# Kernel optimization log

Measured on AMD Instinct MI355X. Metric: run time of the kernel, lower is better.

The kernel has to match this reference:

```python
import jax, jax.numpy as jnp
import numpy as np

WIN = 11      # window_size in pytorch_msssim
SIGMA = 1.5   # gaussian sigma in create_window
LEVELS = 5


def _gauss_window(channels, dtype):
    # 1D gaussian -> normalized 2D window, replicated per channel for depthwise conv
    x = jnp.arange(WIN, dtype=dtype) - WIN // 2
    g = jnp.exp(-(x * x) / (2.0 * SIGMA * SIGMA))
    g = g / jnp.sum(g)
    w2 = jnp.outer(g, g)  # [11,11]
    return jnp.broadcast_to(w2[None, None], (channels, 1, WIN, WIN))


def _dwconv(x, w):
    # depthwise valid conv, NCHW (matches F.conv2d(..., padding=0, groups=channel))
    return jax.lax.conv_general_dilated(
        x, w, window_strides=(1, 1), padding='VALID',
        dimension_numbers=('NCHW', 'OIHW', 'NCHW'),
        feature_group_count=x.shape[1])


def _ssim_cs(p, t, w):
    # pytorch_msssim.ssim with full=True, val_range L=1 (inputs in [0,1])
    C1 = 0.01 ** 2
    C2 = 0.03 ** 2
    mu1 = _dwconv(p, w)
    mu2 = _dwconv(t, w)
    mu1_sq = mu1 * mu1
    mu2_sq = mu2 * mu2
    mu1_mu2 = mu1 * mu2
    sigma1_sq = _dwconv(p * p, w) - mu1_sq
    sigma2_sq = _dwconv(t * t, w) - mu2_sq
    sigma12 = _dwconv(p * t, w) - mu1_mu2
    v1 = 2.0 * sigma12 + C2
    v2 = sigma1_sq + sigma2_sq + C2
    # per-category means (axis 1 = the 10 categories, batched as channels)
    cs = jnp.mean(v1 / v2, axis=(0, 2, 3))                                   # [C]
    sim = jnp.mean(((2.0 * mu1_mu2 + C1) * v1) / ((mu1_sq + mu2_sq + C1) * v2),
                   axis=(0, 2, 3))                                           # [C]
    return sim, cs


def _avg_pool2(x):
    n, c, h, w = x.shape
    return x.reshape(n, c, h // 2, 2, w // 2, 2).mean(axis=(3, 5))


def setup_inputs() -> dict:
    key = jax.random.key(0)
    k1, k2 = jax.random.split(key)
    y_pred = jax.random.uniform(k1, (10, 1024, 1024), dtype=jnp.float32)
    y_true = jax.random.uniform(k2, (10, 1024, 1024), dtype=jnp.float32)
    return {"y_pred": y_pred, "y_true": y_true}


def reference(y_pred, y_true):
    # MSSLoss.forward: loss = sum over 10 categories of msssim(pred[c], true[c]);
    # return 1 - mean(loss)  (loss is a scalar, so mean is identity).
    # All 10 per-category msssim calls are batched as channels of one depthwise conv.
    dtype = y_pred.dtype
    weights = jnp.array([0.0448, 0.2856, 0.3001, 0.2363, 0.1333], dtype=dtype)
    p = y_pred[None]  # [1,10,H,W]
    t = y_true[None]
    w = _gauss_window(p.shape[1], dtype)
    sims, css = [], []
    for _ in range(LEVELS):
        s, c = _ssim_cs(p, t, w)
        sims.append(s)
        css.append(c)
        p = _avg_pool2(p)
        t = _avg_pool2(t)
    mssim = jnp.stack(sims)  # [5, 10]
    mcs = jnp.stack(css)     # [5, 10]
    pow1 = mcs ** weights[:, None]
    pow2 = mssim ** weights[:, None]
    # Po-Hsun-Su pytorch_msssim: output = torch.prod(pow1[:-1] * pow2[-1])
    per_cat = jnp.prod(pow1[:-1] * pow2[-1][None, :], axis=0)  # [10]
    return 1.0 - jnp.sum(per_cat)
```

## Files before the change

### kernel.cpp

```cpp
#include <hip/hip_runtime.h>
#include <cstddef>

#define WIN 11
#define HALO 10
#define NCH 10

typedef float v4f __attribute__((ext_vector_type(4)));

constexpr float Gc[WIN] = {
    0.00102838f, 0.00759876f, 0.03600077f, 0.10936069f, 0.21300554f,
    0.26601173f, 0.21300554f, 0.10936069f, 0.03600077f, 0.00759876f,
    0.00102838f};

constexpr int HPITCH = 33;
constexpr int RS = 76;
constexpr int RSZ = RS * HPITCH;

struct Ptrs {
    const float* p[5];
    const float* t[5];
};

__global__ __launch_bounds__(256) void pool_all(
    const float* __restrict__ P0, const float* __restrict__ T0,
    float* __restrict__ p1, float* __restrict__ t1,
    float* __restrict__ p2, float* __restrict__ t2,
    float* __restrict__ p3, float* __restrict__ t3,
    float* __restrict__ p4, float* __restrict__ t4,
    float* __restrict__ acc) {
    __shared__ float sp2[256], st2[256], sp3[64], st3[64];
    const int tid = threadIdx.x;
    if (blockIdx.x == 0 && tid < 128) acc[tid] = 0.f;

    const int b = blockIdx.x;
    const int bx = b & 15, by = (b >> 4) & 15, ch = b >> 8;
    const int tx = tid & 15, ty = tid >> 4;

    const size_t rbase =
        ((size_t)ch * 1024 + by * 64 + ty * 4) * 1024 + bx * 64 + tx * 4;
    float4 pr[4], tr[4];
#pragma unroll
    for (int r2 = 0; r2 < 4; ++r2) {
        pr[r2] = *(const float4*)(P0 + rbase + (size_t)r2 * 1024);
        tr[r2] = *(const float4*)(T0 + rbase + (size_t)r2 * 1024);
    }
    float p1a = 0.25f * ((pr[0].x + pr[0].y) + (pr[1].x + pr[1].y));
    float p1b = 0.25f * ((pr[0].z + pr[0].w) + (pr[1].z + pr[1].w));
    float p1c = 0.25f * ((pr[2].x + pr[2].y) + (pr[3].x + pr[3].y));
    float p1d = 0.25f * ((pr[2].z + pr[2].w) + (pr[3].z + pr[3].w));
    float t1a = 0.25f * ((tr[0].x + tr[0].y) + (tr[1].x + tr[1].y));
    float t1b = 0.25f * ((tr[0].z + tr[0].w) + (tr[1].z + tr[1].w));
    float t1c = 0.25f * ((tr[2].x + tr[2].y) + (tr[3].x + tr[3].y));
    float t1d = 0.25f * ((tr[2].z + tr[2].w) + (tr[3].z + tr[3].w));
    size_t o1 = ((size_t)ch * 512 + by * 32 + ty * 2) * 512 + bx * 32 + tx * 2;
    *(float2*)(p1 + o1) = make_float2(p1a, p1b);
    *(float2*)(p1 + o1 + 512) = make_float2(p1c, p1d);
    *(float2*)(t1 + o1) = make_float2(t1a, t1b);
    *(float2*)(t1 + o1 + 512) = make_float2(t1c, t1d);
    float p2v = 0.25f * ((p1a + p1b) + (p1c + p1d));
    float t2v = 0.25f * ((t1a + t1b) + (t1c + t1d));
    size_t o2 = ((size_t)ch * 256 + by * 16 + ty) * 256 + bx * 16 + tx;
    p2[o2] = p2v;
    t2[o2] = t2v;
    sp2[tid] = p2v;
    st2[tid] = t2v;
    __syncthreads();
    if (tid < 64) {
        int x3 = tid & 7, y3 = tid >> 3;
        int i0 = (2 * y3) * 16 + 2 * x3;
        float p3v = 0.25f * ((sp2[i0] + sp2[i0 + 1]) + (sp2[i0 + 16] + sp2[i0 + 17]));
        float t3v = 0.25f * ((st2[i0] + st2[i0 + 1]) + (st2[i0 + 16] + st2[i0 + 17]));
        size_t o3 = ((size_t)ch * 128 + by * 8 + y3) * 128 + bx * 8 + x3;
        p3[o3] = p3v;
        t3[o3] = t3v;
        sp3[tid] = p3v;
        st3[tid] = t3v;
    }
    __syncthreads();
    if (tid < 16) {
        int x4 = tid & 3, y4 = tid >> 2;
        int i0 = (2 * y4) * 8 + 2 * x4;
        float p4v = 0.25f * ((sp3[i0] + sp3[i0 + 1]) + (sp3[i0 + 8] + sp3[i0 + 9]));
        float t4v = 0.25f * ((st3[i0] + st3[i0 + 1]) + (st3[i0 + 8] + st3[i0 + 9]));
        size_t o4 = ((size_t)ch * 64 + by * 4 + y4) * 64 + bx * 4 + x4;
        p4[o4] = p4v;
        t4[o4] = t4v;
    }
}

__global__ __launch_bounds__(256) void ssim_strip(Ptrs ptrs,
                                                  float* __restrict__ acc) {
    __shared__ v4f hq[RSZ];
    __shared__ float red[8];

    const int bxi = blockIdx.x;
    int lvl, base;
    if (bxi < 128)      { lvl = 0; base = 0; }
    else if (bxi < 160) { lvl = 1; base = 128; }
    else if (bxi < 168) { lvl = 2; base = 160; }
    else if (bxi < 172) { lvl = 3; base = 168; }
    else                { lvl = 4; base = 172; }
    const int local = bxi - base;
    const int H = 1024 >> lvl;
    const int Wout = H - HALO;
    const int ncol = 32 >> lvl;
    const int cs = local & (ncol - 1);
    const int rsi = local >> (5 - lvl);
    const int X0 = cs * 32;
    const int strip_y0 = rsi * 256;
    const int strip_rows = min(256, Wout - strip_y0);
    const int rows_needed = strip_rows + HALO;
    const int nIter = (strip_rows + 31) >> 5;

    const int c = blockIdx.y;
    const float* Pc = ptrs.p[lvl] + (size_t)c * H * H;
    const float* Tc = ptrs.t[lvl] + (size_t)c * H * H;
    const int tid = threadIdx.x;

    auto load_row18 = [&](int gy, int gxb, float2 lp[9], float2 lt[9]) {
        const float* Pr = Pc + (size_t)gy * H + gxb;
        const float* Tr = Tc + (size_t)gy * H + gxb;
        if (gxb + 18 <= H) {
#pragma unroll
            for (int j = 0; j < 9; ++j) {
                lp[j] = *(const float2*)(Pr + 2 * j);
                lt[j] = *(const float2*)(Tr + 2 * j);
            }
        } else {
#pragma unroll
            for (int j = 0; j < 9; ++j) {
                float2 a = make_float2(0.f, 0.f), b = make_float2(0.f, 0.f);
                if (gxb + 2 * j < H)     { a.x = Pr[2 * j];     b.x = Tr[2 * j]; }
                if (gxb + 2 * j + 1 < H) { a.y = Pr[2 * j + 1]; b.y = Tr[2 * j + 1]; }
                lp[j] = a;
                lt[j] = b;
            }
        }
    };

    auto conv_store8 = [&](int rr, int x0, const float2 lp[9], const float2 lt[9]) {
        v4f aq[8] = {};
#pragma unroll
        for (int xi = 0; xi < 18; ++xi) {
            float pv = (xi & 1) ? lp[xi >> 1].y : lp[xi >> 1].x;
            float tv = (xi & 1) ? lt[xi >> 1].y : lt[xi >> 1].x;
            v4f xq = (v4f){pv, tv, pv * pv + tv * tv, pv * tv};
#pragma unroll
            for (int o = 0; o < 8; ++o) {
                int k = xi - o;
                if (k >= 0 && k <= 10) aq[o] = aq[o] + Gc[k] * xq;
            }
        }
        const int sb = rr * HPITCH + x0;
#pragma unroll
        for (int o = 0; o < 8; ++o) hq[sb + o] = aq[o];
    };

    {
        const int r = tid >> 2, seg = tid & 3;
        if (r < 42) {
            float2 lp[9], lt[9];
            load_row18(strip_y0 + r, X0 + 8 * seg, lp, lt);
            conv_store8(r, 8 * seg, lp, lt);
        }
    }

    const bool isProd = (tid >= 128);
    const int pr = tid & 31;
    const int pseg = (tid >> 5) & 3;
    float2 plp[9], plt[9];
    int prRow = 42 + pr;
    int prSlot = prRow;
    bool pHave = false;
    if (isProd && prRow < rows_needed && nIter > 1) {
        load_row18(strip_y0 + prRow, X0 + 8 * pseg, plp, plt);
        pHave = true;
    }
    __syncthreads();

    float cs_sum = 0.f, sim_sum = 0.f;
    const int txl = tid & 31;
    const int g = (tid >> 5) & 3;
    int y0m = 0;
    for (int i = 0; i < nIter; ++i) {
        if (isProd) {
            if (pHave) conv_store8(prSlot, 8 * pseg, plp, plt);
            prSlot += 32;
            if (prSlot >= RS) prSlot -= RS;
            prRow += 32;
            pHave = (prRow < rows_needed) && (i + 2 < nIter + 1) && (i + 1 < nIter);
            if (pHave) load_row18(strip_y0 + prRow, X0 + 8 * pseg, plp, plt);
        } else {
            int sl = y0m + 8 * g;
            if (sl >= RS) sl -= RS;
            v4f a[8] = {};
#pragma unroll
            for (int yr = 0; yr < 18; ++yr) {
                v4f vq = hq[sl * HPITCH + txl];
#pragma unroll
                for (int o = 0; o < 8; ++o) {
                    int k = yr - o;
                    if (k >= 0 && k <= 10) a[o] = a[o] + Gc[k] * vq;
                }
                ++sl;
                if (sl >= RS) sl = 0;
            }
            const float C1c = 1.0e-4f, C2c = 9.0e-4f;
            const bool colok = (X0 + txl) < Wout;
            const int orow0 = 32 * i + 8 * g;
#pragma unroll
            for (int o = 0; o < 8; ++o) {
                if (colok && (orow0 + o) < strip_rows) {
                    float mu1 = a[o].x, mu2 = a[o].y;
                    float mu1s = mu1 * mu1, mu2s = mu2 * mu2, mu12 = mu1 * mu2;
                    float v2 = a[o].z - mu1s - mu2s + C2c;
                    float v1 = 2.f * (a[o].w - mu12) + C2c;
                    float den2 = mu1s + mu2s + C1c;
                    float num2 = 2.f * mu12 + C1c;
                    float inv = 1.f / (v2 * den2);
                    cs_sum = fmaf(v1 * den2, inv, cs_sum);
                    sim_sum = fmaf(num2 * v1, inv, sim_sum);
                }
            }
        }
        y0m += 32;
        if (y0m >= RS) y0m -= RS;
        __syncthreads();
    }

#pragma unroll
    for (int off = 32; off > 0; off >>= 1) {
        cs_sum += __shfl_down(cs_sum, off, 64);
        sim_sum += __shfl_down(sim_sum, off, 64);
    }
    int wave = tid >> 6;
    if ((tid & 63) == 0) {
        red[wave * 2 + 0] = sim_sum;
        red[wave * 2 + 1] = cs_sum;
    }
    __syncthreads();
    if (tid == 0) {
        float s = red[0] + red[2] + red[4] + red[6];
        float cc = red[1] + red[3] + red[5] + red[7];
        atomicAdd(&acc[(lvl * NCH + c) * 2 + 0], s);
        atomicAdd(&acc[(lvl * NCH + c) * 2 + 1], cc);
    }
}

__global__ void finalize_k(const float* __restrict__ acc, float* __restrict__ out) {
    if (threadIdx.x != 0) return;
    const double w[5] = {0.0448, 0.2856, 0.3001, 0.2363, 0.1333};
    const double counts[5] = {1014.0 * 1014.0, 502.0 * 502.0, 246.0 * 246.0,
                              118.0 * 118.0, 54.0 * 54.0};
    double total = 0.0;
    for (int c = 0; c < NCH; ++c) {
        double pc = 1.0;
        for (int l = 0; l < 4; ++l) {
            double mcs = (double)acc[(l * NCH + c) * 2 + 1] / counts[l];
            pc *= pow(mcs, w[l]);
        }
        double ms4 = (double)acc[(4 * NCH + c) * 2 + 0] / counts[4];
        double p2 = pow(ms4, w[4]);
        pc *= (p2 * p2) * (p2 * p2);
        total += pc;
    }
    *out = (float)(1.0 - total);
}

extern "C" void kernel_launch(void* const* d_in, const int* in_sizes, int n_in,
                              void* d_out, int out_size, void* d_ws, size_t ws_size,
                              hipStream_t stream) {
    const float* P0 = (const float*)d_in[0];
    const float* T0 = (const float*)d_in[1];
    float* out = (float*)d_out;
    float* acc = (float*)d_ws;

    const size_t n1 = (size_t)NCH * 512 * 512;
    const size_t n2 = (size_t)NCH * 256 * 256;
    const size_t n3 = (size_t)NCH * 128 * 128;
    const size_t n4 = (size_t)NCH * 64 * 64;
    float* p1 = acc + 128;
    float* t1 = p1 + n1;
    float* p2 = t1 + n1;
    float* t2 = p2 + n2;
    float* p3 = t2 + n2;
    float* t3 = p3 + n3;
    float* p4 = t3 + n3;
    float* t4 = p4 + n4;

    pool_all<<<2560, 256, 0, stream>>>(P0, T0, p1, t1, p2, t2, p3, t3, p4, t4, acc);

    Ptrs ptrs;
    ptrs.p[0] = P0; ptrs.t[0] = T0;
    ptrs.p[1] = p1; ptrs.t[1] = t1;
    ptrs.p[2] = p2; ptrs.t[2] = t2;
    ptrs.p[3] = p3; ptrs.t[3] = t3;
    ptrs.p[4] = p4; ptrs.t[4] = t4;

    ssim_strip<<<dim3(174, NCH, 1), 256, 0, stream>>>(ptrs, acc);

    finalize_k<<<1, 64, 0, stream>>>(acc, out);
}
```

Measured before the change: 198.0 us.

## Fold finalize into last SSIM block, use fast reciprocal and lighter barrier

Removes the separate finalize kernel launch: each SSIM block bumps an atomic counter, and the last block to finish computes the per-category products and writes the loss. It also replaces the IEEE division with the hardware approximate reciprocal and swaps __syncthreads for an explicit lgkmcnt wait plus s_barrier. These changes save a launch and some ALU and barrier overhead, at the cost of reduced division precision. The counter at acc+112 relies on pool_all zeroing acc on every call.

```diff
diff --git a/kernel.cpp b/kernel.cpp
--- a/kernel.cpp
+++ b/kernel.cpp
@@ -15,6 +15,7 @@
 constexpr int HPITCH = 33;
 constexpr int RS = 76;
 constexpr int RSZ = RS * HPITCH;
+constexpr int NBLK = 174 * NCH;
 
 struct Ptrs {
     const float* p[5];
@@ -89,9 +90,12 @@
 }
 
 __global__ __launch_bounds__(256) void ssim_strip(Ptrs ptrs,
-                                                  float* __restrict__ acc) {
+                                                  float* __restrict__ acc,
+                                                  float* __restrict__ out) {
     __shared__ v4f hq[RSZ];
     __shared__ float red[8];
+    __shared__ double dred[10];
+    __shared__ int isLast;
 
     const int bxi = blockIdx.x;
     int lvl, base;
@@ -217,7 +221,7 @@
                     float v1 = 2.f * (a[o].w - mu12) + C2c;
                     float den2 = mu1s + mu2s + C1c;
                     float num2 = 2.f * mu12 + C1c;
-                    float inv = 1.f / (v2 * den2);
+                    float inv = __builtin_amdgcn_rcpf(v2 * den2);
                     cs_sum = fmaf(v1 * den2, inv, cs_sum);
                     sim_sum = fmaf(num2 * v1, inv, sim_sum);
                 }
@@ -225,7 +229,9 @@
         }
         y0m += 32;
         if (y0m >= RS) y0m -= RS;
-        __syncthreads();
+        asm volatile("s_waitcnt lgkmcnt(0)" ::: "memory");
+        __builtin_amdgcn_s_barrier();
+        __builtin_amdgcn_sched_barrier(0);
     }
 
 #pragma unroll
@@ -244,27 +250,34 @@
         float cc = red[1] + red[3] + red[5] + red[7];
         atomicAdd(&acc[(lvl * NCH + c) * 2 + 0], s);
         atomicAdd(&acc[(lvl * NCH + c) * 2 + 1], cc);
-    }
-}
-
-__global__ void finalize_k(const float* __restrict__ acc, float* __restrict__ out) {
-    if (threadIdx.x != 0) return;
-    const double w[5] = {0.0448, 0.2856, 0.3001, 0.2363, 0.1333};
-    const double counts[5] = {1014.0 * 1014.0, 502.0 * 502.0, 246.0 * 246.0,
-                              118.0 * 118.0, 54.0 * 54.0};
-    double total = 0.0;
-    for (int c = 0; c < NCH; ++c) {
-        double pc = 1.0;
-        for (int l = 0; l < 4; ++l) {
-            double mcs = (double)acc[(l * NCH + c) * 2 + 1] / counts[l];
-            pc *= pow(mcs, w[l]);
-        }
-        double ms4 = (double)acc[(4 * NCH + c) * 2 + 0] / counts[4];
-        double p2 = pow(ms4, w[4]);
-        pc *= (p2 * p2) * (p2 * p2);
-        total += pc;
-    }
-    *out = (float)(1.0 - total);
+        __threadfence();
+        unsigned t = atomicAdd((unsigned int*)acc + 112, 1u);
+        isLast = (t == (unsigned)(NBLK - 1));
+    }
+    __syncthreads();
+
+    if (isLast) {
+        __threadfence();
+        if (tid < 10) {
+            const double w[5] = {0.0448, 0.2856, 0.3001, 0.2363, 0.1333};
+            const double counts[5] = {1014.0 * 1014.0, 502.0 * 502.0,
+                                      246.0 * 246.0, 118.0 * 118.0, 54.0 * 54.0};
+            double pc = 1.0;
+            for (int l = 0; l < 4; ++l) {
+                float v = atomicAdd(&acc[(l * NCH + tid) * 2 + 1], 0.0f);
+                pc *= pow((double)v / counts[l], w[l]);
+            }
+            float s4 = atomicAdd(&acc[(4 * NCH + tid) * 2 + 0], 0.0f);
+            double p2 = pow((double)s4 / counts[4], w[4]);
+            pc *= (p2 * p2) * (p2 * p2);
+            dred[tid] = pc;
+        }
+        if (tid == 0) {
+            double total = 0.0;
+            for (int k = 0; k < 10; ++k) total += dred[k];
+            *out = (float)(1.0 - total);
+        }
+    }
 }
 
 extern "C" void kernel_launch(void* const* d_in, const int* in_sizes, int n_in,
@@ -297,7 +310,5 @@
     ptrs.p[3] = p3; ptrs.t[3] = t3;
     ptrs.p[4] = p4; ptrs.t[4] = t4;
 
-    ssim_strip<<<dim3(174, NCH, 1), 256, 0, stream>>>(ptrs, acc);
-
-    finalize_k<<<1, 64, 0, stream>>>(acc, out);
+    ssim_strip<<<dim3(174, NCH, 1), 256, 0, stream>>>(ptrs, acc, out);
 }
```

Measured after the change: 211.2 us. 6.7% more time.
